# Kernel tuning notes

Measured on AMD Instinct MI355X. Metric: run time of the kernel, lower is better.

Reference implementation:

```python
import jax, jax.numpy as jnp
import numpy as np

NEG_SLOPE = 0.2
MASK_FILL = -9e10


def setup_inputs() -> dict:
    key = jax.random.key(0)
    ks = jax.random.split(key, 8)
    B, N, D = 8, 2048, 64
    return {
        "opes_mask_adj": jax.random.randint(ks[0], (B, N, N), 0, 2, dtype=jnp.int32),
        "opes_mask_job": jax.random.randint(ks[1], (B, N, N), 0, 2, dtype=jnp.int32),
        "batch_idxes": jnp.arange(B, dtype=jnp.int64),
        "feats": jax.random.normal(ks[2], (B, N, D), dtype=jnp.float32),
        "W_ope": jax.random.normal(ks[3], (D, D), dtype=jnp.float32) * (1.0 / np.sqrt(D)),
        "attn_src": jax.random.normal(ks[4], (D,), dtype=jnp.float32) * (1.0 / np.sqrt(D)),
        "attn_dst": jax.random.normal(ks[5], (D,), dtype=jnp.float32) * (1.0 / np.sqrt(D)),
        "lambda_params": jax.random.normal(ks[6], (D, 2), dtype=jnp.float32),
    }


def reference(opes_mask_adj, opes_mask_job, batch_idxes, feats, W_ope, attn_src, attn_dst, lambda_params):
    # h_ope: [B, N, D]  (Linear with weight [out,in]: x @ W^T)
    h_ope = jnp.einsum("bnd,od->bno", feats, W_ope)
    a_src = h_ope @ attn_src  # [B, N]
    a_dst = h_ope @ attn_dst  # [B, N]
    e = a_src[:, :, None] + a_dst[:, None, :]  # [B, N, N]
    e = jnp.where(e >= 0, e, NEG_SLOPE * e)  # leaky relu

    mask_adj = opes_mask_adj[batch_idxes] == 1
    alpha_adj = jax.nn.softmax(jnp.where(mask_adj, e, MASK_FILL), axis=-1)
    h_adj = jnp.einsum("bnm,bmd->bnd", alpha_adj, h_ope)

    mask_job = opes_mask_job[batch_idxes] == 1
    alpha_job = jax.nn.softmax(jnp.where(mask_job, e, MASK_FILL), axis=-1)
    h_job = jnp.einsum("bnm,bmd->bnd", alpha_job, h_ope)

    # in_dim == out_dim -> identity residual (res_fc is None)
    lambdas = jax.nn.softmax(lambda_params, axis=1)  # [D, 2]
    lambda_adj, lambda_job = lambdas[:, 0], lambdas[:, 1]
    return lambda_adj * h_adj + lambda_job * h_job + feats
```

## Files before the change

kernel.cpp:

```cpp
#include <hip/hip_runtime.h>

#define B_ 8
#define N_ 2048
#define D_ 64

typedef __attribute__((ext_vector_type(8))) short bf16x8;
typedef __attribute__((ext_vector_type(4))) float f32x4;

__device__ inline unsigned short f32_bf16_rne(float f) {
    unsigned u = __float_as_uint(f);
    u += 0x7fffu + ((u >> 16) & 1u);
    return (unsigned short)(u >> 16);
}

__device__ inline unsigned cvt_pk_bf16(float lo, float hi) {
    unsigned r;
    asm("v_cvt_pk_bf16_f32 %0, %1, %2" : "=v"(r) : "v"(lo), "v"(hi));
    return r;
}

__global__ __launch_bounds__(256) void prep_kernel(
    const float* __restrict__ feats, const float* __restrict__ W,
    const float* __restrict__ attn_src, const float* __restrict__ attn_dst,
    unsigned short* __restrict__ hT, float* __restrict__ a_src,
    float* __restrict__ F1, float* __restrict__ F2) {
    __shared__ float w_lds[64 * 65];
    __shared__ float f_lds[32 * 64];
    __shared__ unsigned short hT_lds[64 * 40];

    const int t = threadIdx.x;
    const int b = blockIdx.x >> 6;
    const int rowbase = (blockIdx.x & 63) * 32;

#pragma unroll
    for (int k = 0; k < 4; k++) {
        int lin = (k * 256 + t) * 4;
        float4 v = *(const float4*)(W + lin);
        int o = lin >> 6, d = lin & 63;
        float* p = &w_lds[o * 65 + d];
        p[0] = v.x; p[1] = v.y; p[2] = v.z; p[3] = v.w;
    }
#pragma unroll
    for (int k = 0; k < 2; k++) {
        int lin = (k * 256 + t) * 4;
        float4 v = *(const float4*)(feats + (size_t)(b * N_ + rowbase) * D_ + lin);
        float* p = &f_lds[lin];
        p[0] = v.x; p[1] = v.y; p[2] = v.z; p[3] = v.w;
    }
    __syncthreads();

    const int w = t >> 6;
    const int o = t & 63;
    float acc[8] = {0.f, 0.f, 0.f, 0.f, 0.f, 0.f, 0.f, 0.f};
#pragma unroll 8
    for (int d = 0; d < 64; d++) {
        float wv = w_lds[o * 65 + d];
#pragma unroll
        for (int rr = 0; rr < 8; rr++)
            acc[rr] = fmaf(f_lds[(w * 8 + rr) * 64 + d], wv, acc[rr]);
    }
    float as_ = attn_src[o], ad_ = attn_dst[o];
#pragma unroll
    for (int rr = 0; rr < 8; rr++) {
        int row = rowbase + w * 8 + rr;
        float s1 = acc[rr] * as_;
        float s2 = acc[rr] * ad_;
#pragma unroll
        for (int off = 32; off; off >>= 1) {
            s1 += __shfl_xor(s1, off);
            s2 += __shfl_xor(s2, off);
        }
        if (o == 0) {
            a_src[b * N_ + row] = s1;
            F1[b * N_ + row] = __expf(s2);
            F2[b * N_ + row] = __expf(0.2f * s2);
        }
        hT_lds[o * 40 + w * 8 + rr] = f32_bf16_rne(acc[rr]);
    }
    __syncthreads();
    const int d = t >> 2, seg = t & 3;
    uint4 vv = *(const uint4*)(&hT_lds[d * 40 + seg * 8]);
    *(uint4*)(hT + ((size_t)(b * 64 + d) * N_ + rowbase + seg * 8)) = vv;
}

__global__ __launch_bounds__(256, 3) void attn_kernel(
    const int* __restrict__ mask_adj, const int* __restrict__ mask_job,
    const int* __restrict__ batch_idxes,
    const unsigned short* __restrict__ hT, const float* __restrict__ a_src,
    const float* __restrict__ F1, const float* __restrict__ F2,
    const float* __restrict__ feats, const float* __restrict__ lambda_params,
    float* __restrict__ out) {
    __shared__ f32x4 redbuf[3][10][64];

    const int t = threadIdx.x;
    const int b = blockIdx.x >> 7;
    const int rowbase = (blockIdx.x & 127) * 16;
    const int wid = t >> 6, lane = t & 63;
    const int m = lane & 15, q = lane >> 4;
    const int i_a = rowbase + m;

    int bi = batch_idxes[b];
    bi = (bi < 0) ? 0 : ((bi >= B_) ? (B_ - 1) : bi);

    const int jb = wid * 512 + q * 8;
    const int* mA = mask_adj + ((size_t)bi * N_ + i_a) * N_ + jb;
    const int* mJ = mask_job + ((size_t)bi * N_ + i_a) * N_ + jb;
    const float* f1p = F1 + b * N_ + jb;
    const float* f2p = F2 + b * N_ + jb;
    const unsigned short* hp0 = hT + (size_t)b * 64 * N_ + (size_t)m * N_ + jb;
    const unsigned short* hp1 = hp0 + 16 * N_;
    const unsigned short* hp2 = hp0 + 32 * N_;
    const unsigned short* hp3 = hp0 + 48 * N_;

    const float s = a_src[b * N_ + i_a];
    const float cmpT = __expf(-s);
    const float cT = __expf(-0.8f * s);

    f32x4 accA[4], accJ[4], accZA, accZJ;
    const f32x4 z4 = {0.f, 0.f, 0.f, 0.f};
#pragma unroll
    for (int dd = 0; dd < 4; dd++) { accA[dd] = z4; accJ[dd] = z4; }
    accZA = z4; accZJ = z4;
    bf16x8 ones;
#pragma unroll
    for (int i = 0; i < 8; i++) ones[i] = (short)0x3F80;

#pragma unroll
    for (int st = 0; st < 16; st++) {
        const int off = st * 32;
        int4 a0 = *(const int4*)(mA + off);
        int4 a1 = *(const int4*)(mA + off + 4);
        int4 b0 = *(const int4*)(mJ + off);
        int4 b1 = *(const int4*)(mJ + off + 4);
        float4 g0 = *(const float4*)(f1p + off);
        float4 g1 = *(const float4*)(f1p + off + 4);
        float4 h0 = *(const float4*)(f2p + off);
        float4 h1 = *(const float4*)(f2p + off + 4);
        bf16x8 fb0 = *(const bf16x8*)(hp0 + off);
        bf16x8 fb1 = *(const bf16x8*)(hp1 + off);
        bf16x8 fb2 = *(const bf16x8*)(hp2 + off);
        bf16x8 fb3 = *(const bf16x8*)(hp3 + off);

        int ma[8] = {a0.x, a0.y, a0.z, a0.w, a1.x, a1.y, a1.z, a1.w};
        int mj[8] = {b0.x, b0.y, b0.z, b0.w, b1.x, b1.y, b1.z, b1.w};
        float f1v[8] = {g0.x, g0.y, g0.z, g0.w, g1.x, g1.y, g1.z, g1.w};
        float f2v[8] = {h0.x, h0.y, h0.z, h0.w, h1.x, h1.y, h1.z, h1.w};

        unsigned ua[4], uj[4];
#pragma unroll
        for (int wp = 0; wp < 4; wp++) {
            float p0 = (f1v[2 * wp] >= cmpT) ? f1v[2 * wp] : cT * f2v[2 * wp];
            float p1 = (f1v[2 * wp + 1] >= cmpT) ? f1v[2 * wp + 1] : cT * f2v[2 * wp + 1];
            float pa0 = (ma[2 * wp] == 1) ? p0 : 0.f;
            float pa1 = (ma[2 * wp + 1] == 1) ? p1 : 0.f;
            float pj0 = (mj[2 * wp] == 1) ? p0 : 0.f;
            float pj1 = (mj[2 * wp + 1] == 1) ? p1 : 0.f;
            ua[wp] = cvt_pk_bf16(pa0, pa1);
            uj[wp] = cvt_pk_bf16(pj0, pj1);
        }
        union { uint4 u; bf16x8 v; } fa_, fj_;
        fa_.u = make_uint4(ua[0], ua[1], ua[2], ua[3]);
        fj_.u = make_uint4(uj[0], uj[1], uj[2], uj[3]);
        bf16x8 fa = fa_.v, fj = fj_.v;

        accZA = __builtin_amdgcn_mfma_f32_16x16x32_bf16(fa, ones, accZA, 0, 0, 0);
        accZJ = __builtin_amdgcn_mfma_f32_16x16x32_bf16(fj, ones, accZJ, 0, 0, 0);
        accA[0] = __builtin_amdgcn_mfma_f32_16x16x32_bf16(fa, fb0, accA[0], 0, 0, 0);
        accJ[0] = __builtin_amdgcn_mfma_f32_16x16x32_bf16(fj, fb0, accJ[0], 0, 0, 0);
        accA[1] = __builtin_amdgcn_mfma_f32_16x16x32_bf16(fa, fb1, accA[1], 0, 0, 0);
        accJ[1] = __builtin_amdgcn_mfma_f32_16x16x32_bf16(fj, fb1, accJ[1], 0, 0, 0);
        accA[2] = __builtin_amdgcn_mfma_f32_16x16x32_bf16(fa, fb2, accA[2], 0, 0, 0);
        accJ[2] = __builtin_amdgcn_mfma_f32_16x16x32_bf16(fj, fb2, accJ[2], 0, 0, 0);
        accA[3] = __builtin_amdgcn_mfma_f32_16x16x32_bf16(fa, fb3, accA[3], 0, 0, 0);
        accJ[3] = __builtin_amdgcn_mfma_f32_16x16x32_bf16(fj, fb3, accJ[3], 0, 0, 0);
    }

    if (wid) {
#pragma unroll
        for (int c = 0; c < 4; c++) {
            redbuf[wid - 1][c][lane] = accA[c];
            redbuf[wid - 1][4 + c][lane] = accJ[c];
        }
        redbuf[wid - 1][8][lane] = accZA;
        redbuf[wid - 1][9][lane] = accZJ;
    }
    __syncthreads();
    if (wid == 0) {
#pragma unroll
        for (int wv = 0; wv < 3; wv++) {
#pragma unroll
            for (int c = 0; c < 4; c++) {
                accA[c] += redbuf[wv][c][lane];
                accJ[c] += redbuf[wv][4 + c][lane];
            }
            accZA += redbuf[wv][8][lane];
            accZJ += redbuf[wv][9][lane];
        }
        float invA[4], invJ[4];
#pragma unroll
        for (int r = 0; r < 4; r++) {
            invA[r] = 1.f / accZA[r];
            invJ[r] = 1.f / accZJ[r];
        }
#pragma unroll
        for (int dd = 0; dd < 4; dd++) {
            int d = dd * 16 + m;
            float l0 = lambda_params[d * 2];
            float l1 = lambda_params[d * 2 + 1];
            float e0 = __expf(l0), e1 = __expf(l1);
            float inv = 1.f / (e0 + e1);
            float la = e0 * inv, lj = e1 * inv;
#pragma unroll
            for (int r = 0; r < 4; r++) {
                int i = rowbase + q * 4 + r;
                size_t off = (size_t)(b * N_ + i) * D_ + d;
                out[off] = la * accA[dd][r] * invA[r] + lj * accJ[dd][r] * invJ[r] + feats[off];
            }
        }
    }
}

extern "C" void kernel_launch(void* const* d_in, const int* in_sizes, int n_in,
                              void* d_out, int out_size, void* d_ws, size_t ws_size,
                              hipStream_t stream) {
    const int* mask_adj = (const int*)d_in[0];
    const int* mask_job = (const int*)d_in[1];
    const int* batch_idxes = (const int*)d_in[2];
    const float* feats = (const float*)d_in[3];
    const float* W = (const float*)d_in[4];
    const float* attn_src = (const float*)d_in[5];
    const float* attn_dst = (const float*)d_in[6];
    const float* lambda_params = (const float*)d_in[7];
    float* out = (float*)d_out;

    unsigned short* hT = (unsigned short*)d_ws;
    float* a_src = (float*)((char*)d_ws + (size_t)B_ * 64 * N_ * 2);
    float* F1 = a_src + B_ * N_;
    float* F2 = F1 + B_ * N_;

    prep_kernel<<<B_ * (N_ / 32), 256, 0, stream>>>(feats, W, attn_src, attn_dst,
                                                    hT, a_src, F1, F2);
    attn_kernel<<<B_ * (N_ / 16), 256, 0, stream>>>(mask_adj, mask_job, batch_idxes,
                                                    hT, a_src, F1, F2, feats,
                                                    lambda_params, out);
}
```

Before: 312.7 us.

## Pack int32 masks into bitmasks in a pre-pass before attention

New measurement: 342.9 us. 9.6% more time.

```diff
diff --git a/kernel.cpp b/kernel.cpp
--- a/kernel.cpp
+++ b/kernel.cpp
@@ -17,6 +17,31 @@
     unsigned r;
     asm("v_cvt_pk_bf16_f32 %0, %1, %2" : "=v"(r) : "v"(lo), "v"(hi));
     return r;
+}
+
+__global__ __launch_bounds__(256) void pack_kernel(
+    const int* __restrict__ mA, const int* __restrict__ mJ,
+    unsigned char* __restrict__ cA, unsigned char* __restrict__ cJ) {
+    const size_t total = (size_t)B_ * N_ * N_ / 8;
+    const size_t nt = (size_t)gridDim.x * 256;
+    for (size_t g = (size_t)blockIdx.x * 256 + threadIdx.x; g < total; g += nt) {
+        const int* p = mA + g * 8;
+        int4 v0 = *(const int4*)(p);
+        int4 v1 = *(const int4*)(p + 4);
+        unsigned ba = (unsigned)(v0.x == 1) | ((unsigned)(v0.y == 1) << 1) |
+                      ((unsigned)(v0.z == 1) << 2) | ((unsigned)(v0.w == 1) << 3) |
+                      ((unsigned)(v1.x == 1) << 4) | ((unsigned)(v1.y == 1) << 5) |
+                      ((unsigned)(v1.z == 1) << 6) | ((unsigned)(v1.w == 1) << 7);
+        cA[g] = (unsigned char)ba;
+        p = mJ + g * 8;
+        v0 = *(const int4*)(p);
+        v1 = *(const int4*)(p + 4);
+        unsigned bj = (unsigned)(v0.x == 1) | ((unsigned)(v0.y == 1) << 1) |
+                      ((unsigned)(v0.z == 1) << 2) | ((unsigned)(v0.w == 1) << 3) |
+                      ((unsigned)(v1.x == 1) << 4) | ((unsigned)(v1.y == 1) << 5) |
+                      ((unsigned)(v1.z == 1) << 6) | ((unsigned)(v1.w == 1) << 7);
+        cJ[g] = (unsigned char)bj;
+    }
 }
 
 __global__ __launch_bounds__(256) void prep_kernel(
@@ -84,7 +109,7 @@
 }
 
 __global__ __launch_bounds__(256, 3) void attn_kernel(
-    const int* __restrict__ mask_adj, const int* __restrict__ mask_job,
+    const unsigned char* __restrict__ cmA, const unsigned char* __restrict__ cmJ,
     const int* __restrict__ batch_idxes,
     const unsigned short* __restrict__ hT, const float* __restrict__ a_src,
     const float* __restrict__ F1, const float* __restrict__ F2,
@@ -103,8 +128,6 @@
     bi = (bi < 0) ? 0 : ((bi >= B_) ? (B_ - 1) : bi);
 
     const int jb = wid * 512 + q * 8;
-    const int* mA = mask_adj + ((size_t)bi * N_ + i_a) * N_ + jb;
-    const int* mJ = mask_job + ((size_t)bi * N_ + i_a) * N_ + jb;
     const float* f1p = F1 + b * N_ + jb;
     const float* f2p = F2 + b * N_ + jb;
     const unsigned short* hp0 = hT + (size_t)b * 64 * N_ + (size_t)m * N_ + jb;
@@ -112,6 +135,14 @@
     const unsigned short* hp2 = hp0 + 32 * N_;
     const unsigned short* hp3 = hp0 + 48 * N_;
 
+    union { uint4 v[4]; unsigned w[16]; } WA, WJ;
+    {
+        const uint4* pA = (const uint4*)(cmA + ((size_t)bi * N_ + i_a) * (N_ / 8) + wid * 64);
+        const uint4* pJ = (const uint4*)(cmJ + ((size_t)bi * N_ + i_a) * (N_ / 8) + wid * 64);
+        WA.v[0] = pA[0]; WA.v[1] = pA[1]; WA.v[2] = pA[2]; WA.v[3] = pA[3];
+        WJ.v[0] = pJ[0]; WJ.v[1] = pJ[1]; WJ.v[2] = pJ[2]; WJ.v[3] = pJ[3];
+    }
+
     const float s = a_src[b * N_ + i_a];
     const float cmpT = __expf(-s);
     const float cT = __expf(-0.8f * s);
@@ -128,10 +159,6 @@
 #pragma unroll
     for (int st = 0; st < 16; st++) {
         const int off = st * 32;
-        int4 a0 = *(const int4*)(mA + off);
-        int4 a1 = *(const int4*)(mA + off + 4);
-        int4 b0 = *(const int4*)(mJ + off);
-        int4 b1 = *(const int4*)(mJ + off + 4);
         float4 g0 = *(const float4*)(f1p + off);
         float4 g1 = *(const float4*)(f1p + off + 4);
         float4 h0 = *(const float4*)(f2p + off);
@@ -141,20 +168,20 @@
         bf16x8 fb2 = *(const bf16x8*)(hp2 + off);
         bf16x8 fb3 = *(const bf16x8*)(hp3 + off);
 
-        int ma[8] = {a0.x, a0.y, a0.z, a0.w, a1.x, a1.y, a1.z, a1.w};
-        int mj[8] = {b0.x, b0.y, b0.z, b0.w, b1.x, b1.y, b1.z, b1.w};
         float f1v[8] = {g0.x, g0.y, g0.z, g0.w, g1.x, g1.y, g1.z, g1.w};
         float f2v[8] = {h0.x, h0.y, h0.z, h0.w, h1.x, h1.y, h1.z, h1.w};
+        const unsigned byteA = (WA.w[st] >> (q * 8)) & 0xffu;
+        const unsigned byteJ = (WJ.w[st] >> (q * 8)) & 0xffu;
 
         unsigned ua[4], uj[4];
 #pragma unroll
         for (int wp = 0; wp < 4; wp++) {
             float p0 = (f1v[2 * wp] >= cmpT) ? f1v[2 * wp] : cT * f2v[2 * wp];
             float p1 = (f1v[2 * wp + 1] >= cmpT) ? f1v[2 * wp + 1] : cT * f2v[2 * wp + 1];
-            float pa0 = (ma[2 * wp] == 1) ? p0 : 0.f;
-            float pa1 = (ma[2 * wp + 1] == 1) ? p1 : 0.f;
-            float pj0 = (mj[2 * wp] == 1) ? p0 : 0.f;
-            float pj1 = (mj[2 * wp + 1] == 1) ? p1 : 0.f;
+            float pa0 = ((byteA >> (2 * wp)) & 1u) ? p0 : 0.f;
+            float pa1 = ((byteA >> (2 * wp + 1)) & 1u) ? p1 : 0.f;
+            float pj0 = ((byteJ >> (2 * wp)) & 1u) ? p0 : 0.f;
+            float pj1 = ((byteJ >> (2 * wp + 1)) & 1u) ? p1 : 0.f;
             ua[wp] = cvt_pk_bf16(pa0, pa1);
             uj[wp] = cvt_pk_bf16(pj0, pj1);
         }
@@ -237,10 +264,13 @@
     float* a_src = (float*)((char*)d_ws + (size_t)B_ * 64 * N_ * 2);
     float* F1 = a_src + B_ * N_;
     float* F2 = F1 + B_ * N_;
-
+    unsigned char* cmA = (unsigned char*)d_ws + (size_t)B_ * 64 * N_ * 2 + 3 * (size_t)B_ * N_ * 4;
+    unsigned char* cmJ = cmA + (size_t)B_ * N_ * N_ / 8;
+
+    pack_kernel<<<2048, 256, 0, stream>>>(mask_adj, mask_job, cmA, cmJ);
     prep_kernel<<<B_ * (N_ / 32), 256, 0, stream>>>(feats, W, attn_src, attn_dst,
                                                     hT, a_src, F1, F2);
-    attn_kernel<<<B_ * (N_ / 16), 256, 0, stream>>>(mask_adj, mask_job, batch_idxes,
+    attn_kernel<<<B_ * (N_ / 16), 256, 0, stream>>>(cmA, cmJ, batch_idxes,
                                                     hT, a_src, F1, F2, feats,
                                                     lambda_params, out);
 }
```

## Stage mask tiles into LDS with double-buffered global_load_lds prefetch

Applied to the files above, without the earlier changes.

After: 323.5 us. 3.4% more time.

```diff
diff --git a/kernel.cpp b/kernel.cpp
--- a/kernel.cpp
+++ b/kernel.cpp
@@ -90,7 +90,9 @@
     const float* __restrict__ F1, const float* __restrict__ F2,
     const float* __restrict__ feats, const float* __restrict__ lambda_params,
     float* __restrict__ out) {
-    __shared__ f32x4 redbuf[3][10][64];
+    __shared__ int ldsA[4][2][512];
+    __shared__ int ldsJ[4][2][512];
+    __shared__ f32x4 redbuf[3][5][64];
 
     const int t = threadIdx.x;
     const int b = blockIdx.x >> 7;
@@ -102,9 +104,14 @@
     int bi = batch_idxes[b];
     bi = (bi < 0) ? 0 : ((bi >= B_) ? (B_ - 1) : bi);
 
+    const int srow = lane & 15, sgran = lane >> 4;
+    const int* rA = mask_adj + ((size_t)bi * N_ + rowbase + srow) * N_ + wid * 512 + sgran * 4;
+    const int* rJ = mask_job + ((size_t)bi * N_ + rowbase + srow) * N_ + wid * 512 + sgran * 4;
+
+    typedef const __attribute__((address_space(1))) void* gp_t;
+    typedef __attribute__((address_space(3))) void* sp_t;
+
     const int jb = wid * 512 + q * 8;
-    const int* mA = mask_adj + ((size_t)bi * N_ + i_a) * N_ + jb;
-    const int* mJ = mask_job + ((size_t)bi * N_ + i_a) * N_ + jb;
     const float* f1p = F1 + b * N_ + jb;
     const float* f2p = F2 + b * N_ + jb;
     const unsigned short* hp0 = hT + (size_t)b * 64 * N_ + (size_t)m * N_ + jb;
@@ -125,13 +132,32 @@
 #pragma unroll
     for (int i = 0; i < 8; i++) ones[i] = (short)0x3F80;
 
+    auto stage = [&](int tt, int cc) {
+        __builtin_amdgcn_global_load_lds((gp_t)(rA + tt * 32),      (sp_t)&ldsA[wid][cc][0],   16, 0, 0);
+        __builtin_amdgcn_global_load_lds((gp_t)(rA + tt * 32 + 16), (sp_t)&ldsA[wid][cc][256], 16, 0, 0);
+        __builtin_amdgcn_global_load_lds((gp_t)(rJ + tt * 32),      (sp_t)&ldsJ[wid][cc][0],   16, 0, 0);
+        __builtin_amdgcn_global_load_lds((gp_t)(rJ + tt * 32 + 16), (sp_t)&ldsJ[wid][cc][256], 16, 0, 0);
+    };
+
+    stage(0, 0);
+
 #pragma unroll
     for (int st = 0; st < 16; st++) {
+        const int cc = st & 1;
+        if (st < 15) {
+            stage(st + 1, cc ^ 1);
+            asm volatile("s_waitcnt vmcnt(4)" ::: "memory");
+        } else {
+            asm volatile("s_waitcnt vmcnt(0)" ::: "memory");
+        }
+        __builtin_amdgcn_sched_barrier(0);
+
+        const int4 iA0 = *(const int4*)&ldsA[wid][cc][(2 * q) * 64 + m * 4];
+        const int4 iA1 = *(const int4*)&ldsA[wid][cc][(2 * q + 1) * 64 + m * 4];
+        const int4 iJ0 = *(const int4*)&ldsJ[wid][cc][(2 * q) * 64 + m * 4];
+        const int4 iJ1 = *(const int4*)&ldsJ[wid][cc][(2 * q + 1) * 64 + m * 4];
+
         const int off = st * 32;
-        int4 a0 = *(const int4*)(mA + off);
-        int4 a1 = *(const int4*)(mA + off + 4);
-        int4 b0 = *(const int4*)(mJ + off);
-        int4 b1 = *(const int4*)(mJ + off + 4);
         float4 g0 = *(const float4*)(f1p + off);
         float4 g1 = *(const float4*)(f1p + off + 4);
         float4 h0 = *(const float4*)(f2p + off);
@@ -141,8 +167,8 @@
         bf16x8 fb2 = *(const bf16x8*)(hp2 + off);
         bf16x8 fb3 = *(const bf16x8*)(hp3 + off);
 
-        int ma[8] = {a0.x, a0.y, a0.z, a0.w, a1.x, a1.y, a1.z, a1.w};
-        int mj[8] = {b0.x, b0.y, b0.z, b0.w, b1.x, b1.y, b1.z, b1.w};
+        int ma[8] = {iA0.x, iA0.y, iA0.z, iA0.w, iA1.x, iA1.y, iA1.z, iA1.w};
+        int mj[8] = {iJ0.x, iJ0.y, iJ0.z, iJ0.w, iJ1.x, iJ1.y, iJ1.z, iJ1.w};
         float f1v[8] = {g0.x, g0.y, g0.z, g0.w, g1.x, g1.y, g1.z, g1.w};
         float f2v[8] = {h0.x, h0.y, h0.z, h0.w, h1.x, h1.y, h1.z, h1.w};
 
@@ -177,24 +203,31 @@
 
     if (wid) {
 #pragma unroll
-        for (int c = 0; c < 4; c++) {
-            redbuf[wid - 1][c][lane] = accA[c];
-            redbuf[wid - 1][4 + c][lane] = accJ[c];
-        }
-        redbuf[wid - 1][8][lane] = accZA;
-        redbuf[wid - 1][9][lane] = accZJ;
+        for (int c = 0; c < 4; c++) redbuf[wid - 1][c][lane] = accA[c];
+        redbuf[wid - 1][4][lane] = accZA;
     }
     __syncthreads();
     if (wid == 0) {
 #pragma unroll
         for (int wv = 0; wv < 3; wv++) {
 #pragma unroll
-            for (int c = 0; c < 4; c++) {
-                accA[c] += redbuf[wv][c][lane];
-                accJ[c] += redbuf[wv][4 + c][lane];
-            }
-            accZA += redbuf[wv][8][lane];
-            accZJ += redbuf[wv][9][lane];
+            for (int c = 0; c < 4; c++) accA[c] += redbuf[wv][c][lane];
+            accZA += redbuf[wv][4][lane];
+        }
+    }
+    __syncthreads();
+    if (wid) {
+#pragma unroll
+        for (int c = 0; c < 4; c++) redbuf[wid - 1][c][lane] = accJ[c];
+        redbuf[wid - 1][4][lane] = accZJ;
+    }
+    __syncthreads();
+    if (wid == 0) {
+#pragma unroll
+        for (int wv = 0; wv < 3; wv++) {
+#pragma unroll
+            for (int c = 0; c < 4; c++) accJ[c] += redbuf[wv][c][lane];
+            accZJ += redbuf[wv][4][lane];
         }
         float invA[4], invJ[4];
 #pragma unroll
```
